# Kernel optimization log

Hardware: AMD Instinct MI355X
Metric: run time of the kernel (lower is better)

Reference implementation:

```python
import jax, jax.numpy as jnp
import numpy as np

ALPHA = 0.2  # LeakyReLU negative slope


def setup_inputs() -> dict:
    key = jax.random.key(0)
    ks = jax.random.split(key, 7)
    N, D, O, R = 50000, 128, 128, 64
    E1, E2 = 800000, 200000
    return {
        "input": jax.random.normal(ks[0], (N, D), jnp.float32),
        "edge": jax.random.randint(ks[1], (2, E1), 0, N),
        "edge_embed": jax.random.normal(ks[2], (E1, R), jnp.float32),
        "edge_list_nhop": jax.random.randint(ks[3], (2, E2), 0, N),
        "edge_embed_nhop": jax.random.normal(ks[4], (E2, R), jnp.float32),
        "a": jax.random.normal(ks[5], (O, 2 * D + R), jnp.float32) * 0.05,
        "a_2": jax.random.normal(ks[6], (1, O), jnp.float32) * 0.05,
    }


def _gat_forward(x, edge, e_embed, a, a_2):
    N, D = x.shape
    src, dst = edge[0], edge[1]
    # a @ [x_src; x_dst; e_embed]^T computed blockwise (avoids [E, 2D+R] concat)
    a_src, a_dst, a_rel = a[:, :D], a[:, D:2 * D], a[:, 2 * D:]
    edge_m = x[src] @ a_src.T + x[dst] @ a_dst.T + e_embed @ a_rel.T  # [E, O] == edge_m^T
    score = edge_m @ a_2[0]                                            # [E]
    powers = -jnp.where(score > 0, score, ALPHA * score)               # -LeakyReLU
    edge_e = jnp.exp(powers)                                           # [E]
    e_rowsum = jax.ops.segment_sum(edge_e, src, num_segments=N)[:, None]  # [N, 1]
    e_rowsum = jnp.where(e_rowsum == 0.0, 1e-12, e_rowsum)
    edge_w = edge_e[:, None] * edge_m                                  # [E, O]
    h_prime = jax.ops.segment_sum(edge_w, src, num_segments=N)         # [N, O]
    h_prime = h_prime / e_rowsum
    return jax.nn.elu(h_prime)  # concat=True path


def reference(input, edge, edge_embed, edge_list_nhop, edge_embed_nhop, a, a_2):
    edge_all = jnp.concatenate([edge, edge_list_nhop], axis=1)        # [2, E1+E2]
    embed_all = jnp.concatenate([edge_embed, edge_embed_nhop], axis=0)  # [E1+E2, R]
    return _gat_forward(input, edge_all, embed_all, a, a_2)
```

## Files before the change

### kernel.cpp

```cpp
#include <hip/hip_runtime.h>
#include <hip/hip_bf16.h>

#define LRELU_ALPHA 0.2f

typedef __bf16 bf16x8 __attribute__((ext_vector_type(8)));
typedef __bf16 bf16x4 __attribute__((ext_vector_type(4)));
typedef float f32x4 __attribute__((ext_vector_type(4)));

__device__ __forceinline__ float waveReduceSum(float v) {
#pragma unroll
    for (int off = 32; off > 0; off >>= 1)
        v += __shfl_xor(v, off, 64);
    return v;
}

__global__ void k_prep(const float* __restrict__ a, const float* __restrict__ a2,
                       float* __restrict__ vall, __hip_bfloat16* __restrict__ ABf) {
    int idx = blockIdx.x * 256 + threadIdx.x;
    if (idx < 128 * 320) ABf[idx] = __float2bfloat16(a[idx]);
    if (idx < 320) {
        float s = 0.f;
#pragma unroll 8
        for (int o = 0; o < 128; ++o) s += a[o * 320 + idx] * a2[o];
        vall[idx] = s;
    }
}

__global__ void k_node_scores(const float* __restrict__ x, const float* __restrict__ vall,
                              float* __restrict__ s_src, float* __restrict__ s_dst,
                              __hip_bfloat16* __restrict__ XBf, int N) {
    int wid = (int)((blockIdx.x * (size_t)blockDim.x + threadIdx.x) >> 6);
    int lane = threadIdx.x & 63;
    if (wid >= N) return;
    const float* xp = x + (size_t)wid * 128;
    float x0 = xp[lane], x1 = xp[lane + 64];
    XBf[(size_t)wid * 128 + lane]      = __float2bfloat16(x0);
    XBf[(size_t)wid * 128 + 64 + lane] = __float2bfloat16(x1);
    float ps = x0 * vall[lane] + x1 * vall[lane + 64];
    float pd = x0 * vall[128 + lane] + x1 * vall[192 + lane];
    ps = waveReduceSum(ps);
    pd = waveReduceSum(pd);
    if (lane == 0) { s_src[wid] = ps; s_dst[wid] = pd; }
}

__global__ void k_count(const int* __restrict__ e1, int E1, const int* __restrict__ e2, int E2,
                        int* __restrict__ cnt) {
    int e = blockIdx.x * blockDim.x + threadIdx.x;
    if (e >= E1 + E2) return;
    int src = (e < E1) ? e1[e] : e2[e - E1];
    atomicAdd(&cnt[src], 1);
}

__global__ void k_scan1(const int* __restrict__ cnt, int* __restrict__ bsum, int N) {
    __shared__ int red[256];
    int t = threadIdx.x;
    int idx = blockIdx.x * 256 + t;
    red[t] = (idx < N) ? cnt[idx] : 0;
    __syncthreads();
    for (int off = 128; off > 0; off >>= 1) {
        if (t < off) red[t] += red[t + off];
        __syncthreads();
    }
    if (t == 0) bsum[blockIdx.x] = red[0];
}

__global__ void k_scan2(int* __restrict__ bsum, int nb) {
    __shared__ int tmp[256];
    int t = threadIdx.x;
    int v = (t < nb) ? bsum[t] : 0;
    tmp[t] = v;
    __syncthreads();
    for (int off = 1; off < 256; off <<= 1) {
        int add = (t >= off) ? tmp[t - off] : 0;
        __syncthreads();
        tmp[t] += add;
        __syncthreads();
    }
    if (t < nb) bsum[t] = tmp[t] - v;
}

__global__ void k_scan3(const int* __restrict__ cnt, const int* __restrict__ bsum,
                        int* __restrict__ start, int* __restrict__ cursor, int N, int E) {
    __shared__ int tmp[256];
    int t = threadIdx.x;
    int idx = blockIdx.x * 256 + t;
    int v = (idx < N) ? cnt[idx] : 0;
    tmp[t] = v;
    __syncthreads();
    for (int off = 1; off < 256; off <<= 1) {
        int add = (t >= off) ? tmp[t - off] : 0;
        __syncthreads();
        tmp[t] += add;
        __syncthreads();
    }
    if (idx < N) {
        int excl = tmp[t] - v + bsum[blockIdx.x];
        start[idx] = excl;
        cursor[idx] = excl;
    }
    if (blockIdx.x == 0 && t == 0) start[N] = E;
}

__global__ void k_scatter(const int* __restrict__ e1, int E1, const int* __restrict__ e2, int E2,
                          int* __restrict__ cursor, int2* __restrict__ se) {
    int e = blockIdx.x * blockDim.x + threadIdx.x;
    if (e >= E1 + E2) return;
    int src, dst;
    if (e < E1) { src = e1[e]; dst = e1[E1 + e]; }
    else { int t = e - E1; src = e2[t]; dst = e2[E2 + t]; }
    int p = atomicAdd(&cursor[src], 1);
    se[p] = make_int2(dst, e);
}

__global__ void k_gather(const __hip_bfloat16* __restrict__ XBf,
                         const float* __restrict__ emb1, const float* __restrict__ emb2, int E1,
                         const int* __restrict__ start, const int2* __restrict__ se,
                         const float* __restrict__ vall,
                         const float* __restrict__ s_src, const float* __restrict__ s_dst,
                         __hip_bfloat16* __restrict__ G, float* __restrict__ sxf, int N) {
    int n = (int)((blockIdx.x * (size_t)blockDim.x + threadIdx.x) >> 6);
    int lane = threadIdx.x & 63;
    if (n >= N) return;
    n = __builtin_amdgcn_readfirstlane(n);
    int g = lane >> 4;
    int t = lane & 15;
    int b = start[n], en = start[n + 1];
    float ssrc = s_src[n];
    f32x4 r4 = *reinterpret_cast<const f32x4*>(vall + 256 + 4 * t);
    f32x4 w4 = {0.f, 0.f, 0.f, 0.f};
    float u8[8] = {0.f, 0.f, 0.f, 0.f, 0.f, 0.f, 0.f, 0.f};
    float rs = 0.f;

    for (int p = b; p < en; p += 8) {
        int q0 = p + g;
        int q1 = p + 4 + g;
        int c0 = (q0 < en) ? q0 : en - 1;
        int c1 = (q1 < en) ? q1 : en - 1;
        int2 d0 = se[c0];
        int2 d1 = se[c1];
        const float* ep0 = (d0.y < E1) ? emb1 + (size_t)d0.y * 64 : emb2 + (size_t)(d0.y - E1) * 64;
        const float* ep1 = (d1.y < E1) ? emb1 + (size_t)d1.y * 64 : emb2 + (size_t)(d1.y - E1) * 64;
        f32x4 em0 = *reinterpret_cast<const f32x4*>(ep0 + 4 * t);
        f32x4 em1 = *reinterpret_cast<const f32x4*>(ep1 + 4 * t);
        bf16x8 xv0 = *reinterpret_cast<const bf16x8*>(XBf + (size_t)d0.x * 128 + 8 * t);
        bf16x8 xv1 = *reinterpret_cast<const bf16x8*>(XBf + (size_t)d1.x * 128 + 8 * t);
        float sd0 = s_dst[d0.x], sd1 = s_dst[d1.x];
        float t0 = em0.x * r4.x + em0.y * r4.y + em0.z * r4.z + em0.w * r4.w;
        float t1 = em1.x * r4.x + em1.y * r4.y + em1.z * r4.z + em1.w * r4.w;
#pragma unroll
        for (int off = 1; off <= 8; off <<= 1) {
            t0 += __shfl_xor(t0, off, 64);
            t1 += __shfl_xor(t1, off, 64);
        }
        float sc0 = ssrc + sd0 + t0;
        float sc1 = ssrc + sd1 + t1;
        float pz0 = sc0 > 0.f ? sc0 : LRELU_ALPHA * sc0;
        float pz1 = sc1 > 0.f ? sc1 : LRELU_ALPHA * sc1;
        float e0 = __expf(-pz0);
        float e1v = __expf(-pz1);
        if (q0 >= en) e0 = 0.f;
        if (q1 >= en) e1v = 0.f;
        rs += e0 + e1v;
        w4 += e0 * em0 + e1v * em1;
#pragma unroll
        for (int j = 0; j < 8; ++j)
            u8[j] += e0 * (float)xv0[j] + e1v * (float)xv1[j];
    }

#pragma unroll
    for (int j = 0; j < 8; ++j) {
        u8[j] += __shfl_xor(u8[j], 16, 64);
        u8[j] += __shfl_xor(u8[j], 32, 64);
    }
#pragma unroll
    for (int j = 0; j < 4; ++j) {
        w4[j] += __shfl_xor(w4[j], 16, 64);
        w4[j] += __shfl_xor(w4[j], 32, 64);
    }
    rs += __shfl_xor(rs, 16, 64);
    rs += __shfl_xor(rs, 32, 64);

    float inv = (rs == 0.f) ? 0.f : 1.f / rs;
    if (lane < 16) {
        __hip_bfloat16* gp = G + (size_t)n * 192;
        bf16x8 uu;
#pragma unroll
        for (int j = 0; j < 8; ++j) uu[j] = (__bf16)(u8[j] * inv);
        *reinterpret_cast<bf16x8*>(gp + 8 * lane) = uu;
        bf16x4 ww;
#pragma unroll
        for (int j = 0; j < 4; ++j) ww[j] = (__bf16)(w4[j] * inv);
        *reinterpret_cast<bf16x4*>(gp + 128 + 4 * lane) = ww;
        if (lane == 0) sxf[n] = (rs == 0.f) ? 0.f : 1.f;
    }
}

__global__ __launch_bounds__(256) void k_mfma(
    const __hip_bfloat16* __restrict__ XBf, const __hip_bfloat16* __restrict__ G,
    const __hip_bfloat16* __restrict__ ABf, const float* __restrict__ sxf,
    float* __restrict__ out, int N) {
    int lane = threadIdx.x & 63;
    int wave = threadIdx.x >> 6;
    int m0 = blockIdx.x * 64 + wave * 16;
    int q = lane >> 4, m = lane & 15;
    int rowm = m0 + m; if (rowm >= N) rowm = N - 1;
    const __hip_bfloat16* xr = XBf + (size_t)rowm * 128 + q * 8;
    const __hip_bfloat16* gr = G + (size_t)rowm * 192 + q * 8;
    const __hip_bfloat16* br = ABf + (size_t)m * 320 + q * 8;
    f32x4 acc[8];
#pragma unroll
    for (int c = 0; c < 8; ++c) acc[c] = f32x4{0.f, 0.f, 0.f, 0.f};

#pragma unroll
    for (int s = 0; s < 4; ++s) {
        bf16x8 af = *reinterpret_cast<const bf16x8*>(xr + s * 32);
#pragma unroll
        for (int c = 0; c < 8; ++c) {
            bf16x8 bf = *reinterpret_cast<const bf16x8*>(br + (size_t)c * 16 * 320 + s * 32);
            acc[c] = __builtin_amdgcn_mfma_f32_16x16x32_bf16(af, bf, acc[c], 0, 0, 0);
        }
    }
#pragma unroll
    for (int s = 0; s < 6; ++s) {
        bf16x8 af = *reinterpret_cast<const bf16x8*>(gr + s * 32);
#pragma unroll
        for (int c = 0; c < 8; ++c) {
            bf16x8 bf = *reinterpret_cast<const bf16x8*>(br + (size_t)c * 16 * 320 + 128 + s * 32);
            acc[c] = __builtin_amdgcn_mfma_f32_16x16x32_bf16(af, bf, acc[c], 0, 0, 0);
        }
    }

    float sxr[4];
#pragma unroll
    for (int r = 0; r < 4; ++r) {
        int n = m0 + q * 4 + r;
        sxr[r] = (n < N) ? sxf[n] : 0.f;
    }
#pragma unroll
    for (int c = 0; c < 8; ++c) {
#pragma unroll
        for (int r = 0; r < 4; ++r) {
            int n = m0 + q * 4 + r;
            if (n < N) {
                float h = acc[c][r] * sxr[r];
                out[(size_t)n * 128 + c * 16 + m] = h > 0.f ? h : __expf(h) - 1.f;
            }
        }
    }
}

extern "C" void kernel_launch(void* const* d_in, const int* in_sizes, int n_in,
                              void* d_out, int out_size, void* d_ws, size_t ws_size,
                              hipStream_t stream) {
    const float* x    = (const float*)d_in[0];
    const int*   e1   = (const int*)d_in[1];
    const float* emb1 = (const float*)d_in[2];
    const int*   e2   = (const int*)d_in[3];
    const float* emb2 = (const float*)d_in[4];
    const float* a    = (const float*)d_in[5];
    const float* a2   = (const float*)d_in[6];
    float* out = (float*)d_out;

    const int N  = in_sizes[0] / 128;
    const int E1 = in_sizes[1] / 2;
    const int E2 = in_sizes[3] / 2;
    const int E  = E1 + E2;
    const int NB = (N + 255) / 256;

    float* ws    = (float*)d_ws;
    float* vall  = ws;
    __hip_bfloat16* ABf = (__hip_bfloat16*)(ws + 512);
    float* s_src = ws + 512 + 20480;
    float* s_dst = s_src + N;
    float* sxf   = s_dst + N;
    int*   cnt    = (int*)(sxf + N);
    int*   bsum   = cnt + N;
    int*   start  = bsum + 256;
    int*   cursor = start + N + 1;
    size_t so = (size_t)((char*)(cursor + N + 1) - (char*)d_ws);
    so = (so + 15) & ~(size_t)15;
    int2*  se = (int2*)((char*)d_ws + so);
    size_t xo = so + (size_t)E * sizeof(int2);
    xo = (xo + 15) & ~(size_t)15;
    __hip_bfloat16* XBf = (__hip_bfloat16*)((char*)d_ws + xo);
    size_t go = xo + (size_t)N * 128 * sizeof(__hip_bfloat16);
    go = (go + 15) & ~(size_t)15;
    __hip_bfloat16* G = (__hip_bfloat16*)((char*)d_ws + go);

    size_t needed = go + (size_t)N * 192 * sizeof(__hip_bfloat16);
    if (ws_size < needed) return;

    hipMemsetAsync(cnt, 0, (size_t)N * sizeof(int), stream);

    k_prep<<<(128 * 320 + 255) / 256, 256, 0, stream>>>(a, a2, vall, ABf);
    k_node_scores<<<(N * 64 + 255) / 256, 256, 0, stream>>>(x, vall, s_src, s_dst, XBf, N);
    k_count<<<(E + 255) / 256, 256, 0, stream>>>(e1, E1, e2, E2, cnt);
    k_scan1<<<NB, 256, 0, stream>>>(cnt, bsum, N);
    k_scan2<<<1, 256, 0, stream>>>(bsum, NB);
    k_scan3<<<NB, 256, 0, stream>>>(cnt, bsum, start, cursor, N, E);
    k_scatter<<<(E + 255) / 256, 256, 0, stream>>>(e1, E1, e2, E2, cursor, se);
    k_gather<<<(N * 64 + 255) / 256, 256, 0, stream>>>(
        XBf, emb1, emb2, E1, start, se, vall, s_src, s_dst, G, sxf, N);
    k_mfma<<<(N + 63) / 64, 256, 0, stream>>>(XBf, G, ABf, sxf, out, N);
}
```

Before: 557.1 us.

## Fuse count into prep, single-block scan, and software-pipeline gather loads

The edge-count atomics move into the prep kernel, and the three scan kernels become one single-block 1024-thread scan using wave shuffles. Together these remove several launches. The gather loop now software-pipelines the index, embedding and s_dst loads for the next 8 edges while the current batch is computed, to hide latency. The single-block scan serializes about 49 chunks on one CU, and the prefetch raises register pressure.

```diff
diff --git a/kernel.cpp b/kernel.cpp
--- a/kernel.cpp
+++ b/kernel.cpp
@@ -14,8 +14,10 @@
     return v;
 }
 
-__global__ void k_prep(const float* __restrict__ a, const float* __restrict__ a2,
-                       float* __restrict__ vall, __hip_bfloat16* __restrict__ ABf) {
+__global__ void k_prep_count(const float* __restrict__ a, const float* __restrict__ a2,
+                             float* __restrict__ vall, __hip_bfloat16* __restrict__ ABf,
+                             const int* __restrict__ e1, int E1,
+                             const int* __restrict__ e2, int E2, int* __restrict__ cnt) {
     int idx = blockIdx.x * 256 + threadIdx.x;
     if (idx < 128 * 320) ABf[idx] = __float2bfloat16(a[idx]);
     if (idx < 320) {
@@ -23,6 +25,10 @@
 #pragma unroll 8
         for (int o = 0; o < 128; ++o) s += a[o * 320 + idx] * a2[o];
         vall[idx] = s;
+    }
+    if (idx < E1 + E2) {
+        int src = (idx < E1) ? e1[idx] : e2[idx - E1];
+        atomicAdd(&cnt[src], 1);
     }
 }
 
@@ -43,62 +49,43 @@
     if (lane == 0) { s_src[wid] = ps; s_dst[wid] = pd; }
 }
 
-__global__ void k_count(const int* __restrict__ e1, int E1, const int* __restrict__ e2, int E2,
-                        int* __restrict__ cnt) {
-    int e = blockIdx.x * blockDim.x + threadIdx.x;
-    if (e >= E1 + E2) return;
-    int src = (e < E1) ? e1[e] : e2[e - E1];
-    atomicAdd(&cnt[src], 1);
-}
-
-__global__ void k_scan1(const int* __restrict__ cnt, int* __restrict__ bsum, int N) {
-    __shared__ int red[256];
+__global__ __launch_bounds__(1024) void k_scan_all(const int* __restrict__ cnt,
+                                                   int* __restrict__ start,
+                                                   int* __restrict__ cursor, int N) {
+    __shared__ int wsum[16];
     int t = threadIdx.x;
-    int idx = blockIdx.x * 256 + t;
-    red[t] = (idx < N) ? cnt[idx] : 0;
-    __syncthreads();
-    for (int off = 128; off > 0; off >>= 1) {
-        if (t < off) red[t] += red[t + off];
+    int lane = t & 63, wid = t >> 6;
+    int carry = 0;
+    int nch = (N + 1023) / 1024;
+    for (int c = 0; c < nch; ++c) {
+        int idx = c * 1024 + t;
+        int v = (idx < N) ? cnt[idx] : 0;
+        int s = v;
+#pragma unroll
+        for (int off = 1; off < 64; off <<= 1) {
+            int u = __shfl_up(s, off, 64);
+            if (lane >= off) s += u;
+        }
+        if (lane == 63) wsum[wid] = s;
         __syncthreads();
-    }
-    if (t == 0) bsum[blockIdx.x] = red[0];
-}
-
-__global__ void k_scan2(int* __restrict__ bsum, int nb) {
-    __shared__ int tmp[256];
-    int t = threadIdx.x;
-    int v = (t < nb) ? bsum[t] : 0;
-    tmp[t] = v;
-    __syncthreads();
-    for (int off = 1; off < 256; off <<= 1) {
-        int add = (t >= off) ? tmp[t - off] : 0;
+        if (wid == 0) {
+            int ws = (lane < 16) ? wsum[lane] : 0;
+#pragma unroll
+            for (int off = 1; off < 16; off <<= 1) {
+                int u = __shfl_up(ws, off, 64);
+                if (lane >= off) ws += u;
+            }
+            if (lane < 16) wsum[lane] = ws;
+        }
         __syncthreads();
-        tmp[t] += add;
+        int wprefix = (wid == 0) ? 0 : wsum[wid - 1];
+        int total = wsum[15];
+        int excl = s - v + wprefix + carry;
+        if (idx < N) { start[idx] = excl; cursor[idx] = excl; }
         __syncthreads();
-    }
-    if (t < nb) bsum[t] = tmp[t] - v;
-}
-
-__global__ void k_scan3(const int* __restrict__ cnt, const int* __restrict__ bsum,
-                        int* __restrict__ start, int* __restrict__ cursor, int N, int E) {
-    __shared__ int tmp[256];
-    int t = threadIdx.x;
-    int idx = blockIdx.x * 256 + t;
-    int v = (idx < N) ? cnt[idx] : 0;
-    tmp[t] = v;
-    __syncthreads();
-    for (int off = 1; off < 256; off <<= 1) {
-        int add = (t >= off) ? tmp[t - off] : 0;
-        __syncthreads();
-        tmp[t] += add;
-        __syncthreads();
-    }
-    if (idx < N) {
-        int excl = tmp[t] - v + bsum[blockIdx.x];
-        start[idx] = excl;
-        cursor[idx] = excl;
-    }
-    if (blockIdx.x == 0 && t == 0) start[N] = E;
+        carry += total;
+    }
+    if (t == 0) start[N] = carry;
 }
 
 __global__ void k_scatter(const int* __restrict__ e1, int E1, const int* __restrict__ e2, int E2,
@@ -131,40 +118,63 @@
     float u8[8] = {0.f, 0.f, 0.f, 0.f, 0.f, 0.f, 0.f, 0.f};
     float rs = 0.f;
 
-    for (int p = b; p < en; p += 8) {
-        int q0 = p + g;
-        int q1 = p + 4 + g;
-        int c0 = (q0 < en) ? q0 : en - 1;
-        int c1 = (q1 < en) ? q1 : en - 1;
-        int2 d0 = se[c0];
-        int2 d1 = se[c1];
-        const float* ep0 = (d0.y < E1) ? emb1 + (size_t)d0.y * 64 : emb2 + (size_t)(d0.y - E1) * 64;
-        const float* ep1 = (d1.y < E1) ? emb1 + (size_t)d1.y * 64 : emb2 + (size_t)(d1.y - E1) * 64;
-        f32x4 em0 = *reinterpret_cast<const f32x4*>(ep0 + 4 * t);
-        f32x4 em1 = *reinterpret_cast<const f32x4*>(ep1 + 4 * t);
-        bf16x8 xv0 = *reinterpret_cast<const bf16x8*>(XBf + (size_t)d0.x * 128 + 8 * t);
-        bf16x8 xv1 = *reinterpret_cast<const bf16x8*>(XBf + (size_t)d1.x * 128 + 8 * t);
-        float sd0 = s_dst[d0.x], sd1 = s_dst[d1.x];
-        float t0 = em0.x * r4.x + em0.y * r4.y + em0.z * r4.z + em0.w * r4.w;
-        float t1 = em1.x * r4.x + em1.y * r4.y + em1.z * r4.z + em1.w * r4.w;
-#pragma unroll
-        for (int off = 1; off <= 8; off <<= 1) {
-            t0 += __shfl_xor(t0, off, 64);
-            t1 += __shfl_xor(t1, off, 64);
-        }
-        float sc0 = ssrc + sd0 + t0;
-        float sc1 = ssrc + sd1 + t1;
-        float pz0 = sc0 > 0.f ? sc0 : LRELU_ALPHA * sc0;
-        float pz1 = sc1 > 0.f ? sc1 : LRELU_ALPHA * sc1;
-        float e0 = __expf(-pz0);
-        float e1v = __expf(-pz1);
-        if (q0 >= en) e0 = 0.f;
-        if (q1 >= en) e1v = 0.f;
-        rs += e0 + e1v;
-        w4 += e0 * em0 + e1v * em1;
-#pragma unroll
-        for (int j = 0; j < 8; ++j)
-            u8[j] += e0 * (float)xv0[j] + e1v * (float)xv1[j];
+    if (b < en) {
+        f32x4 cem0, cem1;
+        float csd0, csd1;
+        int cd0x, cd1x;
+        {
+            int q0 = b + g, q1 = b + 4 + g;
+            int c0 = (q0 < en) ? q0 : en - 1;
+            int c1 = (q1 < en) ? q1 : en - 1;
+            int2 d0 = se[c0], d1 = se[c1];
+            const float* ep0 = (d0.y < E1) ? emb1 + (size_t)d0.y * 64 : emb2 + (size_t)(d0.y - E1) * 64;
+            const float* ep1 = (d1.y < E1) ? emb1 + (size_t)d1.y * 64 : emb2 + (size_t)(d1.y - E1) * 64;
+            cem0 = *reinterpret_cast<const f32x4*>(ep0 + 4 * t);
+            cem1 = *reinterpret_cast<const f32x4*>(ep1 + 4 * t);
+            csd0 = s_dst[d0.x]; csd1 = s_dst[d1.x];
+            cd0x = d0.x; cd1x = d1.x;
+        }
+        for (int p = b; p < en; p += 8) {
+            f32x4 nem0, nem1;
+            float nsd0, nsd1;
+            int nd0x, nd1x;
+            {
+                int np = p + 8;
+                int q0 = np + g, q1 = np + 4 + g;
+                int c0 = (q0 < en) ? q0 : en - 1;
+                int c1 = (q1 < en) ? q1 : en - 1;
+                int2 d0 = se[c0], d1 = se[c1];
+                const float* ep0 = (d0.y < E1) ? emb1 + (size_t)d0.y * 64 : emb2 + (size_t)(d0.y - E1) * 64;
+                const float* ep1 = (d1.y < E1) ? emb1 + (size_t)d1.y * 64 : emb2 + (size_t)(d1.y - E1) * 64;
+                nem0 = *reinterpret_cast<const f32x4*>(ep0 + 4 * t);
+                nem1 = *reinterpret_cast<const f32x4*>(ep1 + 4 * t);
+                nsd0 = s_dst[d0.x]; nsd1 = s_dst[d1.x];
+                nd0x = d0.x; nd1x = d1.x;
+            }
+            bf16x8 xv0 = *reinterpret_cast<const bf16x8*>(XBf + (size_t)cd0x * 128 + 8 * t);
+            bf16x8 xv1 = *reinterpret_cast<const bf16x8*>(XBf + (size_t)cd1x * 128 + 8 * t);
+            float t0 = cem0.x * r4.x + cem0.y * r4.y + cem0.z * r4.z + cem0.w * r4.w;
+            float t1 = cem1.x * r4.x + cem1.y * r4.y + cem1.z * r4.z + cem1.w * r4.w;
+#pragma unroll
+            for (int off = 1; off <= 8; off <<= 1) {
+                t0 += __shfl_xor(t0, off, 64);
+                t1 += __shfl_xor(t1, off, 64);
+            }
+            float sc0 = ssrc + csd0 + t0;
+            float sc1 = ssrc + csd1 + t1;
+            float pz0 = sc0 > 0.f ? sc0 : LRELU_ALPHA * sc0;
+            float pz1 = sc1 > 0.f ? sc1 : LRELU_ALPHA * sc1;
+            float e0 = __expf(-pz0);
+            float e1v = __expf(-pz1);
+            if (p + g >= en) e0 = 0.f;
+            if (p + 4 + g >= en) e1v = 0.f;
+            rs += e0 + e1v;
+            w4 += e0 * cem0 + e1v * cem1;
+#pragma unroll
+            for (int j = 0; j < 8; ++j)
+                u8[j] += e0 * (float)xv0[j] + e1v * (float)xv1[j];
+            cem0 = nem0; cem1 = nem1; csd0 = nsd0; csd1 = nsd1; cd0x = nd0x; cd1x = nd1x;
+        }
     }
 
 #pragma unroll
@@ -265,7 +275,6 @@
     const int E1 = in_sizes[1] / 2;
     const int E2 = in_sizes[3] / 2;
     const int E  = E1 + E2;
-    const int NB = (N + 255) / 256;
 
     float* ws    = (float*)d_ws;
     float* vall  = ws;
@@ -292,12 +301,10 @@
 
     hipMemsetAsync(cnt, 0, (size_t)N * sizeof(int), stream);
 
-    k_prep<<<(128 * 320 + 255) / 256, 256, 0, stream>>>(a, a2, vall, ABf);
+    int gridPC = ((E > 128 * 320 ? E : 128 * 320) + 255) / 256;
+    k_prep_count<<<gridPC, 256, 0, stream>>>(a, a2, vall, ABf, e1, E1, e2, E2, cnt);
     k_node_scores<<<(N * 64 + 255) / 256, 256, 0, stream>>>(x, vall, s_src, s_dst, XBf, N);
-    k_count<<<(E + 255) / 256, 256, 0, stream>>>(e1, E1, e2, E2, cnt);
-    k_scan1<<<NB, 256, 0, stream>>>(cnt, bsum, N);
-    k_scan2<<<1, 256, 0, stream>>>(bsum, NB);
-    k_scan3<<<NB, 256, 0, stream>>>(cnt, bsum, start, cursor, N, E);
+    k_scan_all<<<1, 1024, 0, stream>>>(cnt, start, cursor, N);
     k_scatter<<<(E + 255) / 256, 256, 0, stream>>>(e1, E1, e2, E2, cursor, se);
     k_gather<<<(N * 64 + 255) / 256, 256, 0, stream>>>(
         XBf, emb1, emb2, E1, start, se, vall, s_src, s_dst, G, sxf, N);
```

Result: slower. 599.4 us (+7.6%).
